# Kernel tuning notes

Measured on AMD Instinct MI355X. Metric: run time of the kernel, lower is better.

## Reference

```python
import jax, jax.numpy as jnp
import numpy as np

EMB_DIM = 1024
N_HEADS = 16

def setup_inputs() -> dict:
    key = jax.random.key(0)
    k1, k2, k3 = jax.random.split(key, 3)
    x = jax.random.normal(k1, (4, 2048, EMB_DIM), dtype=jnp.float32)
    # nn.Linear(emb_dim, 3*emb_dim): weight [3E, E], bias [3E]
    W_qkv = jax.random.normal(k2, (3 * EMB_DIM, EMB_DIM), dtype=jnp.float32) * (EMB_DIM ** -0.5)
    b_qkv = jax.random.normal(k3, (3 * EMB_DIM,), dtype=jnp.float32) * 0.02
    return {"x": x, "W_qkv": W_qkv, "b_qkv": b_qkv}

def reference(x, W_qkv, b_qkv):
    B, T, E = x.shape
    nh, hs = N_HEADS, E // N_HEADS
    qkv = jnp.einsum('bte,fe->btf', x, W_qkv) + b_qkv  # [B,T,3E]
    q, k, v = jnp.split(qkv, 3, axis=-1)
    # [B,T,E] -> [B,nh,T,hs]
    q = q.reshape(B, T, nh, hs).transpose(0, 2, 1, 3)
    k = k.reshape(B, T, nh, hs).transpose(0, 2, 1, 3)
    v = v.reshape(B, T, nh, hs).transpose(0, 2, 1, 3)
    scores = jnp.einsum('bhqd,bhkd->bhqk', q, k) / (hs ** 0.5)
    causal = jnp.tril(jnp.ones((T, T), dtype=bool))
    scores = jnp.where(causal, scores, -jnp.inf)
    attn = jax.nn.softmax(scores, axis=-1)
    out = jnp.einsum('bhqk,bhkd->bhqd', attn, v)
    return out.transpose(0, 2, 1, 3).reshape(B, T, E)
```

## Files before the change

### kernel.cpp

```cpp
#include <hip/hip_runtime.h>
#include <hip/hip_bf16.h>

#define B_   4
#define T_   2048
#define E_   1024
#define NH_  16
#define HS_  64
#define F_   (3 * E_)
#define M_   (B_ * T_)

typedef short bf16x8 __attribute__((ext_vector_type(8)));
typedef float f32x4  __attribute__((ext_vector_type(4)));
typedef float f32x16 __attribute__((ext_vector_type(16)));

__device__ __forceinline__ short f2bf(float f) {
    __hip_bfloat16 h = __float2bfloat16(f);
    return *reinterpret_cast<short*>(&h);
}

__device__ __forceinline__ bf16x8 pack2(float4 a, float4 b) {
    bf16x8 r;
    r[0] = f2bf(a.x); r[1] = f2bf(a.y); r[2] = f2bf(a.z); r[3] = f2bf(a.w);
    r[4] = f2bf(b.x); r[5] = f2bf(b.y); r[6] = f2bf(b.z); r[7] = f2bf(b.w);
    return r;
}

__device__ __forceinline__ unsigned cvtpk(float a, float b) {
    unsigned r;
    asm("v_cvt_pk_bf16_f32 %0, %1, %2" : "=v"(r) : "v"(a), "v"(b));
    return r;
}

__device__ __forceinline__ void gload16(const void* g, void* l) {
    __builtin_amdgcn_global_load_lds(
        (const __attribute__((address_space(1))) unsigned int*)g,
        (__attribute__((address_space(3))) unsigned int*)l, 16, 0, 0);
}

__global__ __launch_bounds__(256) void cvt_bf16(const float* __restrict__ X,
                                                const float* __restrict__ W,
                                                short* __restrict__ Xb,
                                                short* __restrict__ Wb) {
    const long nX = (long)M_ * E_;
    long i = ((long)blockIdx.x * 256 + threadIdx.x) * 8;
    const float* src;
    short* dst;
    long off;
    if (i < nX) { src = X; dst = Xb; off = i; }
    else        { src = W; dst = Wb; off = i - nX; }
    float4 a = *(const float4*)(src + off);
    float4 b = *(const float4*)(src + off + 4);
    *(bf16x8*)(dst + off) = pack2(a, b);
}

#define NT 32

__global__ __launch_bounds__(256, 4) void qkv_gemm_mfma(const short* __restrict__ Xb,
                                                        const short* __restrict__ Wb,
                                                        const float* __restrict__ bias,
                                                        __hip_bfloat16* __restrict__ Qb,
                                                        __hip_bfloat16* __restrict__ Kb,
                                                        __hip_bfloat16* __restrict__ Vf) {
    __shared__ __align__(16) short lds[2 * 8192];

    const int tid = threadIdx.x;
    const int w = tid >> 6, l = tid & 63;
    const int lg = l >> 4, lr = l & 15;
    const int wm = w >> 1, wn = w & 1;

    const int bid = blockIdx.x;
    const int sw = (bid & 7) * 192 + (bid >> 3);
    const int bm = sw / 24, bn = sw % 24;

    const int Rl  = w * 8 + (l >> 3);
    const int cl_ = (l & 7) ^ (Rl & 7);
    const int gr0 = 2 * Rl + (cl_ >> 2);
    const int kc0 = (cl_ & 3) * 8;
    const short* gA = Xb + (long)(bm * 128 + gr0) * E_ + kc0;
    const short* gB = Wb + (long)(bn * 128 + gr0) * E_ + kc0;
    const int dOff = w * 512;

    const f32x4 zero = {0.f, 0.f, 0.f, 0.f};
    f32x4 acc[4][4];
#pragma unroll
    for (int i = 0; i < 4; ++i)
#pragma unroll
        for (int j = 0; j < 4; ++j) acc[i][j] = zero;

#define STAGE(t, p)                                                         \
    {                                                                       \
        const int ko = (t) * 32;                                            \
        short* lb = &lds[(p) * 8192];                                       \
        gload16(gA + ko,                    &lb[dOff]);                     \
        gload16(gA + ko + (long)64 * E_,    &lb[2048 + dOff]);              \
        gload16(gB + ko,                    &lb[4096 + dOff]);              \
        gload16(gB + ko + (long)64 * E_,    &lb[4096 + 2048 + dOff]);       \
    }

    STAGE(0, 0);

    for (int t = 0; t < NT; ++t) {
        const int p = t & 1;
        if (t + 1 < NT) {
            STAGE(t + 1, p ^ 1);
            asm volatile("s_waitcnt vmcnt(4)" ::: "memory");
        } else {
            asm volatile("s_waitcnt vmcnt(0)" ::: "memory");
        }
        __builtin_amdgcn_s_barrier();
        __builtin_amdgcn_sched_barrier(0);

        const short* lA = &lds[p * 8192];
        const short* lB = &lds[p * 8192 + 4096];
        bf16x8 af[4], bf[4];
#pragma unroll
        for (int ng = 0; ng < 4; ++ng) {
            const int R = wn * 32 + ng * 8 + (lr >> 1);
            const int c8 = (lr & 1) * 4 + lg;
            bf[ng] = *(const bf16x8*)&lB[R * 64 + (c8 ^ (R & 7)) * 8];
        }
#pragma unroll
        for (int mg = 0; mg < 4; ++mg) {
            const int R = wm * 32 + mg * 8 + (lr >> 1);
            const int c8 = (lr & 1) * 4 + lg;
            af[mg] = *(const bf16x8*)&lA[R * 64 + (c8 ^ (R & 7)) * 8];
        }

        __builtin_amdgcn_s_setprio(1);
#pragma unroll
        for (int mg = 0; mg < 4; ++mg)
#pragma unroll
            for (int ng = 0; ng < 4; ++ng)
                acc[mg][ng] = __builtin_amdgcn_mfma_f32_16x16x32_bf16(af[mg], bf[ng], acc[mg][ng], 0, 0, 0);
        __builtin_amdgcn_s_setprio(0);
        __builtin_amdgcn_s_barrier();
        __builtin_amdgcn_sched_barrier(0);
    }

    const int sec = bn >> 3;
    const float QSCALE = 0.125f * 1.44269504f;
#pragma unroll
    for (int mg = 0; mg < 4; ++mg)
#pragma unroll
        for (int ng = 0; ng < 4; ++ng) {
            const int row0 = bm * 128 + wm * 64 + mg * 16 + 4 * lg;
            const int col = bn * 128 + wn * 64 + ng * 16 + lr;
            const int cc = col & 1023;
            const int h = cc >> 6, d = cc & 63;
            const int b = row0 >> 11, t0 = row0 & 2047;
            const int bh = b * 16 + h;
            const float bia = bias[col];
            if (sec == 0) {
#pragma unroll
                for (int r = 0; r < 4; ++r)
                    Qb[((long)bh * T_ + t0 + r) * 64 + d] = __float2bfloat16((acc[mg][ng][r] + bia) * QSCALE);
            } else if (sec == 1) {
#pragma unroll
                for (int r = 0; r < 4; ++r)
                    Kb[((long)bh * T_ + t0 + r) * 64 + d] = __float2bfloat16(acc[mg][ng][r] + bia);
            } else {
                const int ktv = t0 >> 6, stv = (t0 >> 5) & 1, ksv = (t0 >> 4) & 1;
                const int hi8 = (t0 >> 3) & 1, j0 = t0 & 7;
                const int lanev = hi8 * 32 + (d & 31);
                const int dtv = d >> 5;
                const long off = (long)bh * 131072 +
                                 ((((((long)ktv * 2 + stv) * 2 + ksv) * 2 + dtv) * 64 + lanev) * 8 + j0);
                uint2 pk;
                pk.x = cvtpk(acc[mg][ng][0] + bia, acc[mg][ng][1] + bia);
                pk.y = cvtpk(acc[mg][ng][2] + bia, acc[mg][ng][3] + bia);
                *(uint2*)((short*)Vf + off) = pk;
            }
        }
#undef STAGE
}

__global__ __launch_bounds__(256, 3) void attn_mfma8(const __hip_bfloat16* __restrict__ Qb,
                                                     const __hip_bfloat16* __restrict__ Kb,
                                                     const __hip_bfloat16* __restrict__ Vf,
                                                     float* __restrict__ out) {
    const int g = blockIdx.x;
    const int xcd = g & 7, kidx = g >> 3;
    const int bh = xcd * 8 + (kidx & 7);
    const int qt = 15 - (kidx >> 3);
    const int b = bh >> 4, h = bh & 15;
    const int tid = threadIdx.x;
    const int wv = tid >> 6, ln = tid & 63;
    const int hi = ln >> 5, q5 = ln & 31;

    __shared__ __align__(16) short kbuf[2 * 8192];

    const short* qbase = (const short*)Qb + (long)bh * T_ * 64;
    const short* kbase = (const short*)Kb + (long)bh * T_ * 64;
    const short* vfrag = (const short*)Vf + (long)bh * 131072;

    const int wq0 = qt * 128 + wv * 32;
    const int qg = wq0 + q5;

    bf16x8 qf[4];
#pragma unroll
    for (int w = 0; w < 4; ++w)
        qf[w] = *(const bf16x8*)&qbase[(long)qg * 64 + w * 16 + hi * 8];

    const int r0 = wv * 8 + (ln >> 3);
    const int cs = (ln & 7) ^ (r0 & 7);
    const short* pK0 = kbase + (long)r0 * 64 + cs * 8;

#define KSTAGE2(kt2, p)                                            \
    {                                                              \
        short* bb = &kbuf[(p) * 8192];                             \
        const long ko = (long)(kt2) * 8192;                        \
        gload16(pK0 + ko,           bb + wv * 512);                \
        gload16(pK0 + ko + 32 * 64, bb + 2048 + wv * 512);         \
        gload16(pK0 + ko + 64 * 64, bb + 4096 + wv * 512);         \
        gload16(pK0 + ko + 96 * 64, bb + 6144 + wv * 512);         \
    }

    const f32x16 zero16 = {0.f,0.f,0.f,0.f, 0.f,0.f,0.f,0.f, 0.f,0.f,0.f,0.f, 0.f,0.f,0.f,0.f};
    f32x16 o0 = zero16, o1 = zero16;
    float lsum = 0.f;

    const int nkt2 = qt + 1;
    KSTAGE2(0, 0);

    for (int kt2 = 0; kt2 < nkt2; ++kt2) {
        const int p = kt2 & 1;
        asm volatile("s_waitcnt vmcnt(0)" ::: "memory");
        __builtin_amdgcn_s_barrier();
        __builtin_amdgcn_sched_barrier(0);
        if (kt2 + 1 < nkt2) KSTAGE2(kt2 + 1, p ^ 1);

#pragma unroll
        for (int half = 0; half < 2; ++half) {
            const int kt = kt2 * 2 + half;
            if (kt * 64 > wq0 + 31) continue;
            const short* K_lds = &kbuf[p * 8192 + half * 4096];
            const bool act1 = (kt * 64 + 32) <= (wq0 + 31);

            const short* vb = vfrag + (long)kt * 4096 + (long)ln * 8;
            bf16x8 vfr[8];
#pragma unroll
            for (int i = 0; i < 8; ++i) vfr[i] = *(const bf16x8*)(vb + i * 512);

            f32x16 sa = zero16, sb = zero16;
            __builtin_amdgcn_s_setprio(1);
#pragma unroll
            for (int w = 0; w < 4; ++w) {
                bf16x8 kf = *(const bf16x8*)&K_lds[q5 * 64 + ((w * 2 + hi) ^ (q5 & 7)) * 8];
                sa = __builtin_amdgcn_mfma_f32_32x32x16_bf16(kf, qf[w], sa, 0, 0, 0);
            }
            if (act1) {
#pragma unroll
                for (int w = 0; w < 4; ++w) {
                    int key = 32 + q5;
                    bf16x8 kf = *(const bf16x8*)&K_lds[key * 64 + ((w * 2 + hi) ^ (key & 7)) * 8];
                    sb = __builtin_amdgcn_mfma_f32_32x32x16_bf16(kf, qf[w], sb, 0, 0, 0);
                }
            }
            __builtin_amdgcn_s_setprio(0);

            if (kt * 64 + 31 > wq0) {
#pragma unroll
                for (int r = 0; r < 16; ++r) {
                    int key = kt * 64 + (r & 3) + 8 * (r >> 2) + 4 * hi;
                    sa[r] = (key <= qg) ? sa[r] : -1e30f;
                }
            }
            if (act1 && (kt * 64 + 63 > wq0)) {
#pragma unroll
                for (int r = 0; r < 16; ++r) {
                    int key = kt * 64 + 32 + (r & 3) + 8 * (r >> 2) + 4 * hi;
                    sb[r] = (key <= qg) ? sb[r] : -1e30f;
                }
            }

            float rs = 0.f;
#pragma unroll
            for (int r = 0; r < 16; ++r) { sa[r] = exp2f(sa[r]); rs += sa[r]; }
            if (act1) {
#pragma unroll
                for (int r = 0; r < 16; ++r) { sb[r] = exp2f(sb[r]); rs += sb[r]; }
            }
            lsum += rs;

            __builtin_amdgcn_s_setprio(1);
#pragma unroll
            for (int st = 0; st < 2; ++st) {
                if (st == 1 && !act1) break;
                const f32x16& s = (st == 0) ? sa : sb;
                unsigned pkv[8];
#pragma unroll
                for (int i = 0; i < 8; ++i) pkv[i] = cvtpk(s[2 * i], s[2 * i + 1]);
#pragma unroll
                for (int ks = 0; ks < 2; ++ks) {
                    unsigned x1 = (unsigned)__shfl_xor((int)(hi ? pkv[4 * ks]     : pkv[4 * ks + 2]), 32, 64);
                    unsigned x2 = (unsigned)__shfl_xor((int)(hi ? pkv[4 * ks + 1] : pkv[4 * ks + 3]), 32, 64);
                    union { unsigned u[4]; bf16x8 v; } fr;
                    fr.u[0] = hi ? x1 : pkv[4 * ks];
                    fr.u[1] = hi ? x2 : pkv[4 * ks + 1];
                    fr.u[2] = hi ? pkv[4 * ks + 2] : x1;
                    fr.u[3] = hi ? pkv[4 * ks + 3] : x2;
                    o0 = __builtin_amdgcn_mfma_f32_32x32x16_bf16(vfr[(st * 2 + ks) * 2],     fr.v, o0, 0, 0, 0);
                    o1 = __builtin_amdgcn_mfma_f32_32x32x16_bf16(vfr[(st * 2 + ks) * 2 + 1], fr.v, o1, 0, 0, 0);
                }
            }
            __builtin_amdgcn_s_setprio(0);
        }
    }
#undef KSTAGE2

    lsum += __shfl_xor(lsum, 32, 64);
    const float inv = 1.f / lsum;
    float* orow = out + ((long)b * T_ + qg) * E_ + h * HS_;
#pragma unroll
    for (int rg = 0; rg < 4; ++rg) {
        float4 v0, v1;
        v0.x = o0[rg * 4 + 0] * inv; v0.y = o0[rg * 4 + 1] * inv;
        v0.z = o0[rg * 4 + 2] * inv; v0.w = o0[rg * 4 + 3] * inv;
        v1.x = o1[rg * 4 + 0] * inv; v1.y = o1[rg * 4 + 1] * inv;
        v1.z = o1[rg * 4 + 2] * inv; v1.w = o1[rg * 4 + 3] * inv;
        *(float4*)&orow[8 * rg + 4 * hi]      = v0;
        *(float4*)&orow[32 + 8 * rg + 4 * hi] = v1;
    }
}

extern "C" void kernel_launch(void* const* d_in, const int* in_sizes, int n_in,
                              void* d_out, int out_size, void* d_ws, size_t ws_size,
                              hipStream_t stream) {
    const float* x     = (const float*)d_in[0];
    const float* W_qkv = (const float*)d_in[1];
    const float* b_qkv = (const float*)d_in[2];
    float* out = (float*)d_out;

    const long per = (long)64 * T_ * 64;
    __hip_bfloat16* Qb = (__hip_bfloat16*)d_ws;
    __hip_bfloat16* Kb = Qb + per;
    __hip_bfloat16* Vf = Kb + per;
    short* Xb = (short*)(Vf + per);
    short* Wb = Xb + (long)M_ * E_;

    const long ncvt = ((long)M_ * E_ + (long)F_ * E_) / 8;
    cvt_bf16<<<(int)(ncvt / 256), 256, 0, stream>>>(x, W_qkv, Xb, Wb);

    qkv_gemm_mfma<<<1536, 256, 0, stream>>>(Xb, Wb, b_qkv, Qb, Kb, Vf);

    attn_mfma8<<<1024, 256, 0, stream>>>(Qb, Kb, Vf, out);
}
```

Before: 140.1 us.

## Enlarge QKV GEMM tile to 256x128 with 512-thread blocks and K=64 stages

The QKV projection GEMM moves from 128x128 tiles with 256 threads and K-step 32 to 256x128 tiles with 512 threads (8 waves) and K-step 64, with the grid halved to 768 blocks. Each wave now computes a 128x32 sub-tile, and the inner loop is split into four sub-phases, each with its own LDS load wait and barrier. The aim is more operand reuse per global load and fewer loop iterations and barriers. In exchange it uses 96KB of LDS, limits occupancy to one block per CU, and adds barriers inside the k-loop.

```diff
diff --git a/kernel.cpp b/kernel.cpp
--- a/kernel.cpp
+++ b/kernel.cpp
@@ -53,98 +53,111 @@
     *(bf16x8*)(dst + off) = pack2(a, b);
 }
 
-#define NT 32
-
-__global__ __launch_bounds__(256, 4) void qkv_gemm_mfma(const short* __restrict__ Xb,
+#define NKT 16
+
+__global__ __launch_bounds__(512, 1) void qkv_gemm_mfma(const short* __restrict__ Xb,
                                                         const short* __restrict__ Wb,
                                                         const float* __restrict__ bias,
                                                         __hip_bfloat16* __restrict__ Qb,
                                                         __hip_bfloat16* __restrict__ Kb,
                                                         __hip_bfloat16* __restrict__ Vf) {
-    __shared__ __align__(16) short lds[2 * 8192];
+    __shared__ __align__(16) short lds[2 * 24576];
 
     const int tid = threadIdx.x;
     const int w = tid >> 6, l = tid & 63;
     const int lg = l >> 4, lr = l & 15;
-    const int wm = w >> 1, wn = w & 1;
+    const int wm = w >> 2, wn = w & 3;
 
     const int bid = blockIdx.x;
-    const int sw = (bid & 7) * 192 + (bid >> 3);
+    const int sw = (bid & 7) * 96 + (bid >> 3);
     const int bm = sw / 24, bn = sw % 24;
 
-    const int Rl  = w * 8 + (l >> 3);
-    const int cl_ = (l & 7) ^ (Rl & 7);
-    const int gr0 = 2 * Rl + (cl_ >> 2);
-    const int kc0 = (cl_ & 3) * 8;
-    const short* gA = Xb + (long)(bm * 128 + gr0) * E_ + kc0;
-    const short* gB = Wb + (long)(bn * 128 + gr0) * E_ + kc0;
-    const int dOff = w * 512;
+    const int Rs  = tid >> 3;
+    const int cls = (tid & 7) ^ (Rs & 7);
+    const int grs = 2 * Rs + (cls >> 2);
+    const int k0s = (cls & 3) * 8;
+    const short* gA0 = Xb + (long)(bm * 256 +       grs) * E_ + k0s;
+    const short* gA1 = Xb + (long)(bm * 256 + 128 + grs) * E_ + k0s;
+    const short* gB0 = Wb + (long)(bn * 128 +       grs) * E_ + k0s;
+    const int dW = w * 512;
 
     const f32x4 zero = {0.f, 0.f, 0.f, 0.f};
-    f32x4 acc[4][4];
-#pragma unroll
-    for (int i = 0; i < 4; ++i)
-#pragma unroll
-        for (int j = 0; j < 4; ++j) acc[i][j] = zero;
-
-#define STAGE(t, p)                                                         \
-    {                                                                       \
-        const int ko = (t) * 32;                                            \
-        short* lb = &lds[(p) * 8192];                                       \
-        gload16(gA + ko,                    &lb[dOff]);                     \
-        gload16(gA + ko + (long)64 * E_,    &lb[2048 + dOff]);              \
-        gload16(gB + ko,                    &lb[4096 + dOff]);              \
-        gload16(gB + ko + (long)64 * E_,    &lb[4096 + 2048 + dOff]);       \
+    f32x4 acc[8][2];
+#pragma unroll
+    for (int i = 0; i < 8; ++i) { acc[i][0] = zero; acc[i][1] = zero; }
+
+#define STAGE(t, p)                                                          \
+    {                                                                        \
+        const int ko = (t) * 64;                                             \
+        short* lb = &lds[(p) * 24576];                                       \
+        gload16(gA0 + ko,      lb + 0 * 4096 + dW);                          \
+        gload16(gA1 + ko,      lb + 1 * 4096 + dW);                          \
+        gload16(gA0 + ko + 32, lb + 2 * 4096 + dW);                          \
+        gload16(gA1 + ko + 32, lb + 3 * 4096 + dW);                          \
+        gload16(gB0 + ko,      lb + 16384 + 0 * 4096 + dW);                  \
+        gload16(gB0 + ko + 32, lb + 16384 + 1 * 4096 + dW);                  \
     }
 
     STAGE(0, 0);
 
-    for (int t = 0; t < NT; ++t) {
+    for (int t = 0; t < NKT; ++t) {
         const int p = t & 1;
-        if (t + 1 < NT) {
+        if (t + 1 < NKT) {
             STAGE(t + 1, p ^ 1);
-            asm volatile("s_waitcnt vmcnt(4)" ::: "memory");
+            asm volatile("s_waitcnt vmcnt(6)" ::: "memory");
         } else {
             asm volatile("s_waitcnt vmcnt(0)" ::: "memory");
         }
         __builtin_amdgcn_s_barrier();
         __builtin_amdgcn_sched_barrier(0);
 
-        const short* lA = &lds[p * 8192];
-        const short* lB = &lds[p * 8192 + 4096];
-        bf16x8 af[4], bf[4];
-#pragma unroll
-        for (int ng = 0; ng < 4; ++ng) {
-            const int R = wn * 32 + ng * 8 + (lr >> 1);
-            const int c8 = (lr & 1) * 4 + lg;
-            bf[ng] = *(const bf16x8*)&lB[R * 64 + (c8 ^ (R & 7)) * 8];
-        }
-#pragma unroll
-        for (int mg = 0; mg < 4; ++mg) {
-            const int R = wm * 32 + mg * 8 + (lr >> 1);
-            const int c8 = (lr & 1) * 4 + lg;
-            af[mg] = *(const bf16x8*)&lA[R * 64 + (c8 ^ (R & 7)) * 8];
-        }
-
-        __builtin_amdgcn_s_setprio(1);
-#pragma unroll
-        for (int mg = 0; mg < 4; ++mg)
-#pragma unroll
-            for (int ng = 0; ng < 4; ++ng)
-                acc[mg][ng] = __builtin_amdgcn_mfma_f32_16x16x32_bf16(af[mg], bf[ng], acc[mg][ng], 0, 0, 0);
-        __builtin_amdgcn_s_setprio(0);
-        __builtin_amdgcn_s_barrier();
-        __builtin_amdgcn_sched_barrier(0);
+        const short* lbuf = &lds[p * 24576];
+        const int c8 = (lr & 1) * 4 + lg;
+
+        bf16x8 bf[2][2];
+#pragma unroll
+        for (int ng = 0; ng < 2; ++ng) {
+            const int Rb = wn * 16 + ng * 8 + (lr >> 1);
+#pragma unroll
+            for (int kk = 0; kk < 2; ++kk)
+                bf[ng][kk] = *(const bf16x8*)&lbuf[16384 + kk * 4096 + Rb * 64 + (c8 ^ (Rb & 7)) * 8];
+        }
+
+#pragma unroll
+        for (int q = 0; q < 4; ++q) {
+            bf16x8 af[2][2];
+#pragma unroll
+            for (int m2 = 0; m2 < 2; ++m2) {
+                const int mg = q * 2 + m2;
+                const int Ra = mg * 8 + (lr >> 1);
+#pragma unroll
+                for (int kk = 0; kk < 2; ++kk)
+                    af[m2][kk] = *(const bf16x8*)&lbuf[(kk * 2 + wm) * 4096 + Ra * 64 + (c8 ^ (Ra & 7)) * 8];
+            }
+            asm volatile("s_waitcnt lgkmcnt(0)" ::: "memory");
+            __builtin_amdgcn_sched_barrier(0);
+            __builtin_amdgcn_s_setprio(1);
+#pragma unroll
+            for (int m2 = 0; m2 < 2; ++m2)
+#pragma unroll
+                for (int ng = 0; ng < 2; ++ng) {
+                    acc[q * 2 + m2][ng] = __builtin_amdgcn_mfma_f32_16x16x32_bf16(af[m2][0], bf[ng][0], acc[q * 2 + m2][ng], 0, 0, 0);
+                    acc[q * 2 + m2][ng] = __builtin_amdgcn_mfma_f32_16x16x32_bf16(af[m2][1], bf[ng][1], acc[q * 2 + m2][ng], 0, 0, 0);
+                }
+            __builtin_amdgcn_s_setprio(0);
+            __builtin_amdgcn_s_barrier();
+            __builtin_amdgcn_sched_barrier(0);
+        }
     }
 
     const int sec = bn >> 3;
     const float QSCALE = 0.125f * 1.44269504f;
 #pragma unroll
-    for (int mg = 0; mg < 4; ++mg)
-#pragma unroll
-        for (int ng = 0; ng < 4; ++ng) {
-            const int row0 = bm * 128 + wm * 64 + mg * 16 + 4 * lg;
-            const int col = bn * 128 + wn * 64 + ng * 16 + lr;
+    for (int mg = 0; mg < 8; ++mg)
+#pragma unroll
+        for (int ng = 0; ng < 2; ++ng) {
+            const int row0 = bm * 256 + wm * 128 + mg * 16 + 4 * lg;
+            const int col = bn * 128 + wn * 32 + ng * 16 + lr;
             const int cc = col & 1023;
             const int h = cc >> 6, d = cc & 63;
             const int b = row0 >> 11, t0 = row0 & 2047;
@@ -341,7 +354,7 @@
     const long ncvt = ((long)M_ * E_ + (long)F_ * E_) / 8;
     cvt_bf16<<<(int)(ncvt / 256), 256, 0, stream>>>(x, W_qkv, Xb, Wb);
 
-    qkv_gemm_mfma<<<1536, 256, 0, stream>>>(Xb, Wb, b_qkv, Qb, Kb, Vf);
+    qkv_gemm_mfma<<<768, 512, 0, stream>>>(Xb, Wb, b_qkv, Qb, Kb, Vf);
 
     attn_mfma8<<<1024, 256, 0, stream>>>(Qb, Kb, Vf, out);
 }
```

New measurement: 146.2 us. +4.4%, slower.

## Enlarge QKV GEMM tile to 256x128 and restructure prefetch to single barrier

Applied to the files above, without the earlier changes.

The QKV projection GEMM now computes a 256x128 output tile per block instead of 128x128, halving the grid and doubling each warp's accumulator rows. This makes each loaded B fragment serve twice as many MFMAs, cutting LDS and global traffic per flop. The pipeline also changes: it waits for all loads, does one barrier, then issues the next stage's prefetch before computing, which removes the trailing barrier. The costs are more registers (occupancy drops to 2 blocks per SM), a larger LDS footprint, and fewer blocks to balance across CUs.

```diff
diff --git a/kernel.cpp b/kernel.cpp
--- a/kernel.cpp
+++ b/kernel.cpp
@@ -55,13 +55,13 @@
 
 #define NT 32
 
-__global__ __launch_bounds__(256, 4) void qkv_gemm_mfma(const short* __restrict__ Xb,
+__global__ __launch_bounds__(256, 2) void qkv_gemm_mfma(const short* __restrict__ Xb,
                                                         const short* __restrict__ Wb,
                                                         const float* __restrict__ bias,
                                                         __hip_bfloat16* __restrict__ Qb,
                                                         __hip_bfloat16* __restrict__ Kb,
                                                         __hip_bfloat16* __restrict__ Vf) {
-    __shared__ __align__(16) short lds[2 * 8192];
+    __shared__ __align__(16) short lds[2 * 12288];
 
     const int tid = threadIdx.x;
     const int w = tid >> 6, l = tid & 63;
@@ -69,81 +69,74 @@
     const int wm = w >> 1, wn = w & 1;
 
     const int bid = blockIdx.x;
-    const int sw = (bid & 7) * 192 + (bid >> 3);
+    const int sw = (bid & 7) * 96 + (bid >> 3);
     const int bm = sw / 24, bn = sw % 24;
 
-    const int Rl  = w * 8 + (l >> 3);
-    const int cl_ = (l & 7) ^ (Rl & 7);
-    const int gr0 = 2 * Rl + (cl_ >> 2);
-    const int kc0 = (cl_ & 3) * 8;
-    const short* gA = Xb + (long)(bm * 128 + gr0) * E_ + kc0;
-    const short* gB = Wb + (long)(bn * 128 + gr0) * E_ + kc0;
+    const int Rs  = tid >> 3;
+    const int cls = (tid & 7) ^ (Rs & 7);
+    const int gr1 = 2 * Rs + (cls >> 2);
+    const int k0s = (cls & 3) * 8;
+    const short* gA = Xb + (long)(bm * 256 + gr1) * E_ + k0s;
+    const short* gB = Wb + (long)(bn * 128 + gr1) * E_ + k0s;
     const int dOff = w * 512;
 
     const f32x4 zero = {0.f, 0.f, 0.f, 0.f};
-    f32x4 acc[4][4];
-#pragma unroll
-    for (int i = 0; i < 4; ++i)
+    f32x4 acc[8][4];
+#pragma unroll
+    for (int i = 0; i < 8; ++i)
 #pragma unroll
         for (int j = 0; j < 4; ++j) acc[i][j] = zero;
 
-#define STAGE(t, p)                                                         \
-    {                                                                       \
-        const int ko = (t) * 32;                                            \
-        short* lb = &lds[(p) * 8192];                                       \
-        gload16(gA + ko,                    &lb[dOff]);                     \
-        gload16(gA + ko + (long)64 * E_,    &lb[2048 + dOff]);              \
-        gload16(gB + ko,                    &lb[4096 + dOff]);              \
-        gload16(gB + ko + (long)64 * E_,    &lb[4096 + 2048 + dOff]);       \
+#define STAGE(t, p)                                                   \
+    {                                                                 \
+        const int ko = (t) * 32;                                      \
+        short* lb = &lds[(p) * 12288];                                \
+        gload16(gA + ko,                  &lb[dOff]);                 \
+        gload16(gA + ko + (long) 64 * E_, &lb[2048 + dOff]);          \
+        gload16(gA + ko + (long)128 * E_, &lb[4096 + dOff]);          \
+        gload16(gA + ko + (long)192 * E_, &lb[4096 + 2048 + dOff]);   \
+        gload16(gB + ko,                  &lb[8192 + dOff]);          \
+        gload16(gB + ko + (long) 64 * E_, &lb[8192 + 2048 + dOff]);   \
     }
 
     STAGE(0, 0);
 
     for (int t = 0; t < NT; ++t) {
         const int p = t & 1;
-        if (t + 1 < NT) {
-            STAGE(t + 1, p ^ 1);
-            asm volatile("s_waitcnt vmcnt(4)" ::: "memory");
-        } else {
-            asm volatile("s_waitcnt vmcnt(0)" ::: "memory");
-        }
+        asm volatile("s_waitcnt vmcnt(0)" ::: "memory");
         __builtin_amdgcn_s_barrier();
         __builtin_amdgcn_sched_barrier(0);
-
-        const short* lA = &lds[p * 8192];
-        const short* lB = &lds[p * 8192 + 4096];
-        bf16x8 af[4], bf[4];
+        if (t + 1 < NT) STAGE(t + 1, p ^ 1);
+
+        const short* lA = &lds[p * 12288 + wm * 4096];
+        const short* lB = &lds[p * 12288 + 8192];
+        const int c8 = (lr & 1) * 4 + lg;
+
+        bf16x8 bf[4];
 #pragma unroll
         for (int ng = 0; ng < 4; ++ng) {
             const int R = wn * 32 + ng * 8 + (lr >> 1);
-            const int c8 = (lr & 1) * 4 + lg;
             bf[ng] = *(const bf16x8*)&lB[R * 64 + (c8 ^ (R & 7)) * 8];
         }
-#pragma unroll
-        for (int mg = 0; mg < 4; ++mg) {
-            const int R = wm * 32 + mg * 8 + (lr >> 1);
-            const int c8 = (lr & 1) * 4 + lg;
-            af[mg] = *(const bf16x8*)&lA[R * 64 + (c8 ^ (R & 7)) * 8];
+        __builtin_amdgcn_s_setprio(1);
+#pragma unroll
+        for (int mg = 0; mg < 8; ++mg) {
+            const int R = mg * 8 + (lr >> 1);
+            bf16x8 af = *(const bf16x8*)&lA[R * 64 + (c8 ^ (R & 7)) * 8];
+#pragma unroll
+            for (int ng = 0; ng < 4; ++ng)
+                acc[mg][ng] = __builtin_amdgcn_mfma_f32_16x16x32_bf16(af, bf[ng], acc[mg][ng], 0, 0, 0);
         }
-
-        __builtin_amdgcn_s_setprio(1);
-#pragma unroll
-        for (int mg = 0; mg < 4; ++mg)
-#pragma unroll
-            for (int ng = 0; ng < 4; ++ng)
-                acc[mg][ng] = __builtin_amdgcn_mfma_f32_16x16x32_bf16(af[mg], bf[ng], acc[mg][ng], 0, 0, 0);
         __builtin_amdgcn_s_setprio(0);
-        __builtin_amdgcn_s_barrier();
-        __builtin_amdgcn_sched_barrier(0);
     }
 
     const int sec = bn >> 3;
     const float QSCALE = 0.125f * 1.44269504f;
 #pragma unroll
-    for (int mg = 0; mg < 4; ++mg)
+    for (int mg = 0; mg < 8; ++mg)
 #pragma unroll
         for (int ng = 0; ng < 4; ++ng) {
-            const int row0 = bm * 128 + wm * 64 + mg * 16 + 4 * lg;
+            const int row0 = bm * 256 + wm * 128 + mg * 16 + 4 * lg;
             const int col = bn * 128 + wn * 64 + ng * 16 + lr;
             const int cc = col & 1023;
             const int h = cc >> 6, d = cc & 63;
@@ -341,7 +334,7 @@
     const long ncvt = ((long)M_ * E_ + (long)F_ * E_) / 8;
     cvt_bf16<<<(int)(ncvt / 256), 256, 0, stream>>>(x, W_qkv, Xb, Wb);
 
-    qkv_gemm_mfma<<<1536, 256, 0, stream>>>(Xb, Wb, b_qkv, Qb, Kb, Vf);
+    qkv_gemm_mfma<<<768, 256, 0, stream>>>(Xb, Wb, b_qkv, Qb, Kb, Vf);
 
     attn_mfma8<<<1024, 256, 0, stream>>>(Qb, Kb, Vf, out);
 }
```

New measurement: 128.9 us. 1.09x faster.
